# Performance work log

Hardware: AMD Instinct MI355X
Metric: run time of the kernel (lower is better)

## Reference

```python
import jax, jax.numpy as jnp
import numpy as np

NUM_HEADS = 8


def setup_inputs() -> dict:
    key = jax.random.key(0)
    ks = jax.random.split(key, 5)
    B, N, D = 2, 2048, 512
    scale = 1.0 / np.sqrt(D)  # xavier-ish init for stability
    return {
        "x": jax.random.normal(ks[0], (B, N, D), dtype=jnp.float32),
        "Wq": jax.random.normal(ks[1], (D, D), dtype=jnp.float32) * scale,
        "Wk": jax.random.normal(ks[2], (D, D), dtype=jnp.float32) * scale,
        "Wv": jax.random.normal(ks[3], (D, D), dtype=jnp.float32) * scale,
        "Wo": jax.random.normal(ks[4], (D, D), dtype=jnp.float32) * scale,
        "log_c": jnp.zeros((), dtype=jnp.float32),
        "log_beta": jnp.zeros((), dtype=jnp.float32),
    }


def reference(x, Wq, Wk, Wv, Wo, log_c, log_beta):
    B, N, D = x.shape
    H = NUM_HEADS
    dh = D // H

    # torch nn.Linear: y = x @ W.T
    def proj(W):
        return (x @ W.T).reshape(B, N, H, dh).transpose(0, 2, 1, 3)  # [B,H,N,dh]

    q, k, v = proj(Wq), proj(Wk), proj(Wv)

    c = jax.nn.softplus(log_c)
    beta = jax.nn.softplus(log_beta) + 0.5

    q_nsq = jnp.sum(q * q, axis=-1)  # [B,H,N]
    k_nsq = jnp.sum(k * k, axis=-1)  # [B,H,N]
    qk = jnp.einsum("bhnd,bhmd->bhnm", q, k)  # [B,H,N,N]

    diff_sq = jnp.maximum(q_nsq[..., :, None] - 2.0 * qk + k_nsq[..., None, :], 0.0)
    hyp_factor = jnp.sqrt(1.0 + c * (q_nsq[..., :, None] + k_nsq[..., None, :]))
    dist = jnp.sqrt(diff_sq + 1e-8) * hyp_factor
    scores = -beta * dist

    # causal mask (original: causal = mask is not None)
    causal = jnp.tril(jnp.ones((N, N), dtype=bool))
    scores = jnp.where(causal, scores, -jnp.inf)

    p = jax.nn.softmax(scores, axis=-1)
    out = jnp.einsum("bhnm,bhmd->bhnd", p, v)  # [B,H,N,dh]
    out = out.transpose(0, 2, 1, 3).reshape(B, N, D)
    return out @ Wo.T
```

## Files before the change

kernel.cpp:

```cpp
#include <hip/hip_runtime.h>
#include <math.h>

#define BB   2
#define NN   2048
#define DDIM 512
#define HH   8
#define DH   64
#define MTOT (BB*NN)
#define LDK  72
#define EE   (BB*HH*NN*DH)
#define WN   (DDIM*DDIM)
#define NSLOT (BB*HH*32*4)

typedef __attribute__((ext_vector_type(8))) short bf16x8;
typedef __attribute__((ext_vector_type(4))) float f32x4;

__device__ __forceinline__ float softplus_f(float x) {
    return x > 20.f ? x : log1pf(expf(x));
}
__device__ __forceinline__ unsigned short f2bf(float x) {
    union { float f; unsigned u; } v; v.f = x;
    unsigned r = v.u + 0x7fffu + ((v.u >> 16) & 1u);
    return (unsigned short)(r >> 16);
}
__device__ __forceinline__ float bf2f(unsigned short h) {
    union { unsigned u; float f; } v; v.u = ((unsigned)h) << 16; return v.f;
}

__global__ __launch_bounds__(256)
void split_hl(const float* __restrict__ x,  const float* __restrict__ Wq,
              const float* __restrict__ Wk, const float* __restrict__ Wv,
              const float* __restrict__ Wo,
              unsigned short* __restrict__ xh,  unsigned short* __restrict__ xl,
              unsigned short* __restrict__ wqh, unsigned short* __restrict__ wql,
              unsigned short* __restrict__ wkh, unsigned short* __restrict__ wkl,
              unsigned short* __restrict__ wvh, unsigned short* __restrict__ wvl,
              unsigned short* __restrict__ woh, unsigned short* __restrict__ wol)
{
    const float* src; unsigned short *dh, *dl; int nq;
    switch (blockIdx.y) {
        case 0:  src = x;  dh = xh;  dl = xl;  nq = EE / 4; break;
        case 1:  src = Wq; dh = wqh; dl = wql; nq = WN / 4; break;
        case 2:  src = Wk; dh = wkh; dl = wkl; nq = WN / 4; break;
        case 3:  src = Wv; dh = wvh; dl = wvl; nq = WN / 4; break;
        default: src = Wo; dh = woh; dl = wol; nq = WN / 4; break;
    }
    for (int i = blockIdx.x * 256 + threadIdx.x; i < nq; i += gridDim.x * 256) {
        float4 v = *(const float4*)(src + 4 * (size_t)i);
        ushort4 h, l;
        h.x = f2bf(v.x); l.x = f2bf(v.x - bf2f(h.x));
        h.y = f2bf(v.y); l.y = f2bf(v.y - bf2f(h.y));
        h.z = f2bf(v.z); l.z = f2bf(v.z - bf2f(h.z));
        h.w = f2bf(v.w); l.w = f2bf(v.w - bf2f(h.w));
        *(ushort4*)(dh + 4 * (size_t)i) = h;
        *(ushort4*)(dl + 4 * (size_t)i) = l;
    }
}

__global__ __launch_bounds__(256, 3)
void mm_mfma(const unsigned short* __restrict__ Ahg, const unsigned short* __restrict__ Alg,
             const unsigned short* __restrict__ W0h, const unsigned short* __restrict__ W0l,
             const unsigned short* __restrict__ W1h, const unsigned short* __restrict__ W1l,
             const unsigned short* __restrict__ W2h, const unsigned short* __restrict__ W2l,
             const int is_out,
             unsigned short* __restrict__ Qhi, unsigned short* __restrict__ Qlo,
             unsigned short* __restrict__ Khi, unsigned short* __restrict__ Klo,
             unsigned short* __restrict__ Vb, float* __restrict__ Outp,
             float* __restrict__ QN, float* __restrict__ KN)
{
    const int mode = is_out ? 3 : (int)blockIdx.z;
    const unsigned short* Wh = (mode == 1) ? W1h : ((mode == 2) ? W2h : W0h);
    const unsigned short* Wl = (mode == 1) ? W1l : ((mode == 2) ? W2l : W0l);
    const int m0 = blockIdx.x * 64, n0 = blockIdx.y * 128;

    __shared__ unsigned short Ah_s[4 * 64 * 8];
    __shared__ unsigned short Al_s[4 * 64 * 8];
    __shared__ unsigned short Bh_s[4 * 128 * 8];
    __shared__ unsigned short Bl_s[4 * 128 * 8];

    const int tid  = threadIdx.x;
    const int lane = tid & 63, lx = lane & 15, q4 = lane >> 4;
    const int w = tid >> 6, wm = w & 1, wn = w >> 1;
    const int rowA = tid & 63,  kqA = tid >> 6;
    const int rowB = tid & 127, kb  = tid >> 7;

    f32x4 acc[2][4];
    #pragma unroll
    for (int mt = 0; mt < 2; ++mt)
        #pragma unroll
        for (int nt = 0; nt < 4; ++nt)
            acc[mt][nt] = (f32x4){0.f, 0.f, 0.f, 0.f};

    const int am = m0 + rowA;
    const int ab = am >> 11, an = am & 2047;
    const size_t brow = (size_t)(n0 + rowB) * DDIM;

    uint4 rah, ral, rbh0, rbh1, rbl0, rbl1;
    {
        const int e = kqA * 8;
        size_t aoff = (mode == 3)
            ? ((((size_t)(ab * HH + (e >> 6)) * NN + an) << 6) + (e & 63))
            : ((size_t)am * DDIM + e);
        rah = *(const uint4*)(Ahg + aoff);
        ral = *(const uint4*)(Alg + aoff);
        const int eb = kb * 8;
        rbh0 = *(const uint4*)(Wh + brow + eb);
        rbh1 = *(const uint4*)(Wh + brow + eb + 16);
        rbl0 = *(const uint4*)(Wl + brow + eb);
        rbl1 = *(const uint4*)(Wl + brow + eb + 16);
    }

    for (int k0 = 0; k0 < DDIM; k0 += 32) {
        __syncthreads();
        *(uint4*)&Ah_s[(kqA << 9) + (rowA << 3)] = rah;
        *(uint4*)&Al_s[(kqA << 9) + (rowA << 3)] = ral;
        *(uint4*)&Bh_s[(kb << 10) + (rowB << 3)]       = rbh0;
        *(uint4*)&Bh_s[((kb + 2) << 10) + (rowB << 3)] = rbh1;
        *(uint4*)&Bl_s[(kb << 10) + (rowB << 3)]       = rbl0;
        *(uint4*)&Bl_s[((kb + 2) << 10) + (rowB << 3)] = rbl1;
        __syncthreads();

        if (k0 + 32 < DDIM) {
            const int e = k0 + 32 + kqA * 8;
            size_t aoff = (mode == 3)
                ? ((((size_t)(ab * HH + (e >> 6)) * NN + an) << 6) + (e & 63))
                : ((size_t)am * DDIM + e);
            rah = *(const uint4*)(Ahg + aoff);
            ral = *(const uint4*)(Alg + aoff);
            const int eb = k0 + 32 + kb * 8;
            rbh0 = *(const uint4*)(Wh + brow + eb);
            rbh1 = *(const uint4*)(Wh + brow + eb + 16);
            rbl0 = *(const uint4*)(Wl + brow + eb);
            rbl1 = *(const uint4*)(Wl + brow + eb + 16);
        }

        bf16x8 fah[2], fal[2], fbh[4], fbl[4];
        #pragma unroll
        for (int mt = 0; mt < 2; ++mt) {
            const int off = (q4 << 9) + ((wm * 32 + mt * 16 + lx) << 3);
            fah[mt] = *(const bf16x8*)&Ah_s[off];
            fal[mt] = *(const bf16x8*)&Al_s[off];
        }
        #pragma unroll
        for (int nt = 0; nt < 4; ++nt) {
            const int off = (q4 << 10) + ((wn * 64 + nt * 16 + lx) << 3);
            fbh[nt] = *(const bf16x8*)&Bh_s[off];
            fbl[nt] = *(const bf16x8*)&Bl_s[off];
        }
        #pragma unroll
        for (int mt = 0; mt < 2; ++mt)
            #pragma unroll
            for (int nt = 0; nt < 4; ++nt) {
                acc[mt][nt] = __builtin_amdgcn_mfma_f32_16x16x32_bf16(fah[mt], fbh[nt], acc[mt][nt], 0, 0, 0);
                acc[mt][nt] = __builtin_amdgcn_mfma_f32_16x16x32_bf16(fah[mt], fbl[nt], acc[mt][nt], 0, 0, 0);
                acc[mt][nt] = __builtin_amdgcn_mfma_f32_16x16x32_bf16(fal[mt], fbh[nt], acc[mt][nt], 0, 0, 0);
            }
    }

    if (mode == 0 || mode == 1) {
        float* Np = (mode == 0) ? QN : KN;
        const int head = (n0 + wn * 64) >> 6;
        #pragma unroll
        for (int mt = 0; mt < 2; ++mt)
            #pragma unroll
            for (int r = 0; r < 4; ++r) {
                float s = 0.f;
                #pragma unroll
                for (int nt = 0; nt < 4; ++nt) s = fmaf(acc[mt][nt][r], acc[mt][nt][r], s);
                s += __shfl_xor(s, 1);
                s += __shfl_xor(s, 2);
                s += __shfl_xor(s, 4);
                s += __shfl_xor(s, 8);
                if (lx == 0) {
                    const int m = m0 + wm * 32 + mt * 16 + q4 * 4 + r;
                    Np[(size_t)((m >> 11) * HH + head) * NN + (m & 2047)] = s;
                }
            }
    }

    #pragma unroll
    for (int mt = 0; mt < 2; ++mt) {
        #pragma unroll
        for (int r = 0; r < 4; ++r) {
            const int m = m0 + wm * 32 + mt * 16 + q4 * 4 + r;
            const int b = m >> 11, n2 = m & 2047;
            #pragma unroll
            for (int nt = 0; nt < 4; ++nt) {
                const int j = n0 + wn * 64 + nt * 16 + lx;
                const float v = acc[mt][nt][r];
                if (mode == 3) {
                    Outp[(size_t)m * DDIM + j] = v;
                } else {
                    const size_t idx = (((size_t)(b * HH + (j >> 6)) * NN + n2) << 6) + (j & 63);
                    if (mode == 2) {
                        Vb[idx] = f2bf(v);
                    } else {
                        const unsigned short h = f2bf(v);
                        const unsigned short l = f2bf(v - bf2f(h));
                        if (mode == 0) { Qhi[idx] = h; Qlo[idx] = l; }
                        else           { Khi[idx] = h; Klo[idx] = l; }
                    }
                }
            }
        }
    }
}

__global__ __launch_bounds__(256)
void v_transpose(const unsigned short* __restrict__ Vb, unsigned short* __restrict__ Vt)
{
    __shared__ unsigned short T[64 * LDK];
    const int id = blockIdx.x;
    const int bh = id >> 5, nt = id & 31;
    const size_t ibase = (((size_t)bh * NN + nt * 64) << 6);
    const int row = threadIdx.x >> 2, ch = threadIdx.x & 3;

    #pragma unroll
    for (int half = 0; half < 2; ++half) {
        const int col = ch * 8 + half * 32;
        *(uint4*)&T[row * LDK + col] = *(const uint4*)(Vb + ibase + (row << 6) + col);
    }
    __syncthreads();

    const size_t obase = (size_t)bh * 64 * NN;
    #pragma unroll
    for (int half = 0; half < 2; ++half) {
        const int col = ch * 8 + half * 32;
        union { unsigned short u[8]; uint4 v; } tmp;
        #pragma unroll
        for (int j = 0; j < 8; ++j) tmp.u[j] = T[(col + j) * LDK + row];
        *(uint4*)(Vt + obase + (size_t)row * NN + nt * 64 + col) = tmp.v;
    }
}

__global__ __launch_bounds__(256, 4)
void attn_mfma(const unsigned short* __restrict__ Qhi, const unsigned short* __restrict__ Qlo,
               const unsigned short* __restrict__ Khi, const unsigned short* __restrict__ Klo,
               const unsigned short* __restrict__ Vt,
               const float* __restrict__ QN, const float* __restrict__ KN,
               const float* __restrict__ pLC, const float* __restrict__ pLB,
               float* __restrict__ Opart, float* __restrict__ Mp, float* __restrict__ Lp)
{
    __shared__ unsigned short Kh_s[8 * 64 * 8];
    __shared__ unsigned short Kl_s[8 * 64 * 8];
    __shared__ unsigned short Vt_s[8 * 64 * 8];
    __shared__ unsigned short P_s [8 * 64 * 8];
    __shared__ float kn_s[64];
    __shared__ float qn_s[64];

    const int idx = blockIdx.x;
    const int g   = (idx >= 48) ? 3 : (idx >= 24) ? 2 : (idx >= 8) ? 1 : 0;
    const int rem = idx - 4 * g * (g + 1);
    const int C   = g + 1;
    const int qt  = g * 8 + rem / C;
    const int c0  = rem % C;
    const int bh  = blockIdx.y;
    const int nk  = qt + 1;
    const int kt0  = (c0 * nk) / C;
    const int kend = ((c0 + 1) * nk) / C;

    const int tid  = threadIdx.x;
    const int w    = tid >> 6;
    const int lane = tid & 63;
    const int lx   = lane & 15;
    const int q4   = lane >> 4;

    const float hc    = softplus_f(pLC[0]);
    const float betaL = (softplus_f(pLB[0]) + 0.5f) * 1.44269504f;

    const size_t base = ((size_t)bh * NN) << 6;

    union { unsigned short u[8]; bf16x8 v; } ones_u;
    #pragma unroll
    for (int j = 0; j < 8; ++j) ones_u.u[j] = 0x3F80;
    const bf16x8 ones = ones_u.v;

    const unsigned short* qrh = Qhi + base + ((size_t)(qt * 64 + w * 16 + lx) << 6) + q4 * 8;
    const unsigned short* qrl = Qlo + base + ((size_t)(qt * 64 + w * 16 + lx) << 6) + q4 * 8;
    const bf16x8 qh0 = *(const bf16x8*)(qrh);
    const bf16x8 qh1 = *(const bf16x8*)(qrh + 32);
    const bf16x8 ql0 = *(const bf16x8*)(qrl);
    const bf16x8 ql1 = *(const bf16x8*)(qrl + 32);

    if (tid < 64) qn_s[tid] = QN[(size_t)bh * NN + qt * 64 + tid];

    f32x4 Oacc[4];
    f32x4 Lacc = (f32x4){0.f, 0.f, 0.f, 0.f};
    float m_st[4];
    #pragma unroll
    for (int r = 0; r < 4; ++r) {
        m_st[r] = -INFINITY;
        Oacc[r] = (f32x4){0.f, 0.f, 0.f, 0.f};
    }

    const int srow = tid >> 2, sch = tid & 3;

    uint4 pKh0, pKh1, pKl0, pKl1, pVt0, pVt1; float pkn = 0.f;
    {
        const unsigned short* kh = Khi + base + ((size_t)(kt0 * 64 + srow) << 6);
        const unsigned short* kl = Klo + base + ((size_t)(kt0 * 64 + srow) << 6);
        const unsigned short* vt = Vt  + base + (size_t)srow * NN + kt0 * 64;
        pKh0 = *(const uint4*)(kh + sch * 8);  pKh1 = *(const uint4*)(kh + sch * 8 + 32);
        pKl0 = *(const uint4*)(kl + sch * 8);  pKl1 = *(const uint4*)(kl + sch * 8 + 32);
        pVt0 = *(const uint4*)(vt + sch * 8);  pVt1 = *(const uint4*)(vt + sch * 8 + 32);
        if (tid < 64) pkn = KN[(size_t)bh * NN + kt0 * 64 + tid];
    }

    __syncthreads();

    for (int kt = kt0; kt < kend; ++kt) {
        *(uint4*)&Kh_s[(sch << 9) + (srow << 3)]       = pKh0;
        *(uint4*)&Kh_s[((sch + 4) << 9) + (srow << 3)] = pKh1;
        *(uint4*)&Kl_s[(sch << 9) + (srow << 3)]       = pKl0;
        *(uint4*)&Kl_s[((sch + 4) << 9) + (srow << 3)] = pKl1;
        *(uint4*)&Vt_s[(sch << 9) + (srow << 3)]       = pVt0;
        *(uint4*)&Vt_s[((sch + 4) << 9) + (srow << 3)] = pVt1;
        if (tid < 64) kn_s[tid] = pkn;
        __syncthreads();

        if (kt + 1 < kend) {
            const unsigned short* kh = Khi + base + ((size_t)((kt + 1) * 64 + srow) << 6);
            const unsigned short* kl = Klo + base + ((size_t)((kt + 1) * 64 + srow) << 6);
            const unsigned short* vt = Vt  + base + (size_t)srow * NN + (kt + 1) * 64;
            pKh0 = *(const uint4*)(kh + sch * 8);  pKh1 = *(const uint4*)(kh + sch * 8 + 32);
            pKl0 = *(const uint4*)(kl + sch * 8);  pKl1 = *(const uint4*)(kl + sch * 8 + 32);
            pVt0 = *(const uint4*)(vt + sch * 8);  pVt1 = *(const uint4*)(vt + sch * 8 + 32);
            if (tid < 64) pkn = KN[(size_t)bh * NN + (kt + 1) * 64 + tid];
        }

        f32x4 S[4];
        #pragma unroll
        for (int t = 0; t < 4; ++t) {
            f32x4 acc = (f32x4){0.f, 0.f, 0.f, 0.f};
            #pragma unroll
            for (int c2 = 0; c2 < 2; ++c2) {
                const int off = ((c2 * 4 + q4) << 9) + (t << 7) + (lx << 3);
                const bf16x8 kh = *(const bf16x8*)&Kh_s[off];
                const bf16x8 kl = *(const bf16x8*)&Kl_s[off];
                const bf16x8 qh = c2 ? qh1 : qh0;
                const bf16x8 ql = c2 ? ql1 : ql0;
                acc = __builtin_amdgcn_mfma_f32_16x16x32_bf16(qh, kh, acc, 0, 0, 0);
                acc = __builtin_amdgcn_mfma_f32_16x16x32_bf16(qh, kl, acc, 0, 0, 0);
                acc = __builtin_amdgcn_mfma_f32_16x16x32_bf16(ql, kh, acc, 0, 0, 0);
            }
            S[t] = acc;
        }

        float qn_r[4];
        #pragma unroll
        for (int r = 0; r < 4; ++r) qn_r[r] = qn_s[w * 16 + q4 * 4 + r];
        const bool diag = (kt == qt);

        float mrow[4] = {-INFINITY, -INFINITY, -INFINITY, -INFINITY};
        #pragma unroll
        for (int t = 0; t < 4; ++t) {
            const float kn = kn_s[t * 16 + lx];
            #pragma unroll
            for (int r = 0; r < 4; ++r) {
                const float sumn = qn_r[r] + kn;
                float diff = fmaxf(fmaf(-2.f, S[t][r], sumn), 0.f);
                float s = -betaL * sqrtf(fmaf(hc, sumn, 1.f) * (diff + 1e-8f));
                const int cc = t * 16 + lx;
                const int rr = w * 16 + q4 * 4 + r;
                if (diag && cc > rr) s = -INFINITY;
                S[t][r] = s;
                mrow[r] = fmaxf(mrow[r], s);
            }
        }

        #pragma unroll
        for (int r = 0; r < 4; ++r) {
            float m = mrow[r];
            m = fmaxf(m, __shfl_xor(m, 1));
            m = fmaxf(m, __shfl_xor(m, 2));
            m = fmaxf(m, __shfl_xor(m, 4));
            m = fmaxf(m, __shfl_xor(m, 8));
            const float mn = fmaxf(m_st[r], m);
            const float al = exp2f(m_st[r] - mn);
            m_st[r] = mn;
            const int prow = ((w * 16 + q4 * 4 + r) << 3) + (lx & 7);
            #pragma unroll
            for (int t = 0; t < 4; ++t) {
                const float p = exp2f(S[t][r] - mn);
                P_s[((t * 2 + (lx >> 3)) << 9) + prow] = f2bf(p);
                Oacc[t][r] *= al;
            }
            Lacc[r] *= al;
        }

        __builtin_amdgcn_wave_barrier();

        #pragma unroll
        for (int c2 = 0; c2 < 2; ++c2) {
            const bf16x8 pa = *(const bf16x8*)&P_s[((c2 * 4 + q4) << 9) + ((w * 16 + lx) << 3)];
            #pragma unroll
            for (int t = 0; t < 4; ++t) {
                const bf16x8 vb = *(const bf16x8*)&Vt_s[((c2 * 4 + q4) << 9) + (t << 7) + (lx << 3)];
                Oacc[t] = __builtin_amdgcn_mfma_f32_16x16x32_bf16(pa, vb, Oacc[t], 0, 0, 0);
            }
            Lacc = __builtin_amdgcn_mfma_f32_16x16x32_bf16(pa, ones, Lacc, 0, 0, 0);
        }
        __syncthreads();
    }

    const int slot = ((bh * 32 + qt) << 2) + c0;
    float* op = Opart + ((size_t)slot << 12);
    #pragma unroll
    for (int r = 0; r < 4; ++r) {
        const int row = w * 16 + q4 * 4 + r;
        #pragma unroll
        for (int t = 0; t < 4; ++t)
            op[row * 64 + t * 16 + lx] = Oacc[t][r];
        if (lx == 0) {
            Mp[slot * 64 + row] = m_st[r];
            Lp[slot * 64 + row] = Lacc[r];
        }
    }
}

__global__ __launch_bounds__(256)
void attn_combine(const float* __restrict__ Opart, const float* __restrict__ Mp,
                  const float* __restrict__ Lp,
                  unsigned short* __restrict__ AOh, unsigned short* __restrict__ AOl)
{
    const int bh = blockIdx.x >> 5, qt = blockIdx.x & 31;
    const int C = (qt >> 3) + 1;
    const int row = threadIdx.x >> 2, qd = threadIdx.x & 3;
    const int slot0 = (bh * 32 + qt) << 2;

    float m = -INFINITY;
    for (int c = 0; c < C; ++c) m = fmaxf(m, Mp[(slot0 + c) * 64 + row]);
    float L = 0.f;
    float o[16];
    #pragma unroll
    for (int j = 0; j < 16; ++j) o[j] = 0.f;

    for (int c = 0; c < C; ++c) {
        const float wgt = exp2f(Mp[(slot0 + c) * 64 + row] - m);
        L += wgt * Lp[(slot0 + c) * 64 + row];
        const float* op = Opart + (((size_t)(slot0 + c)) << 12) + row * 64 + qd * 16;
        #pragma unroll
        for (int j4 = 0; j4 < 4; ++j4) {
            float4 v = *(const float4*)(op + j4 * 4);
            o[j4*4+0] = fmaf(wgt, v.x, o[j4*4+0]);
            o[j4*4+1] = fmaf(wgt, v.y, o[j4*4+1]);
            o[j4*4+2] = fmaf(wgt, v.z, o[j4*4+2]);
            o[j4*4+3] = fmaf(wgt, v.w, o[j4*4+3]);
        }
    }

    const float inv = 1.f / L;
    const size_t obase = (((size_t)bh * NN + qt * 64 + row) << 6) + qd * 16;
    union { unsigned short u[8]; uint4 v; } h2[2], l2[2];
    #pragma unroll
    for (int j = 0; j < 16; ++j) {
        const float ov = o[j] * inv;
        const unsigned short h = f2bf(ov);
        const unsigned short l = f2bf(ov - bf2f(h));
        h2[j >> 3].u[j & 7] = h;
        l2[j >> 3].u[j & 7] = l;
    }
    *(uint4*)(AOh + obase)     = h2[0].v;
    *(uint4*)(AOh + obase + 8) = h2[1].v;
    *(uint4*)(AOl + obase)     = l2[0].v;
    *(uint4*)(AOl + obase + 8) = l2[1].v;
}

extern "C" void kernel_launch(void* const* d_in, const int* in_sizes, int n_in,
                              void* d_out, int out_size, void* d_ws, size_t ws_size,
                              hipStream_t stream)
{
    const float* x        = (const float*)d_in[0];
    const float* Wq       = (const float*)d_in[1];
    const float* Wk       = (const float*)d_in[2];
    const float* Wv       = (const float*)d_in[3];
    const float* Wo       = (const float*)d_in[4];
    const float* log_c    = (const float*)d_in[5];
    const float* log_beta = (const float*)d_in[6];
    float* out = (float*)d_out;

    unsigned short* p = (unsigned short*)d_ws;
    unsigned short* xh  = p;            p += EE;
    unsigned short* xl  = p;            p += EE;
    unsigned short* wqh = p;            p += WN;
    unsigned short* wql = p;            p += WN;
    unsigned short* wkh = p;            p += WN;
    unsigned short* wkl = p;            p += WN;
    unsigned short* wvh = p;            p += WN;
    unsigned short* wvl = p;            p += WN;
    unsigned short* woh = p;            p += WN;
    unsigned short* wol = p;            p += WN;
    unsigned short* Qhi = p;            p += EE;
    unsigned short* Qlo = p;            p += EE;
    unsigned short* Khi = p;            p += EE;
    unsigned short* Klo = p;            p += EE;
    unsigned short* Vb  = p;            p += EE;
    unsigned short* Vtr = p;            p += EE;
    unsigned short* AOh = p;            p += EE;
    unsigned short* AOl = p;            p += EE;
    float* QN    = (float*)p;
    float* KN    = QN + (size_t)BB * HH * NN;
    float* Opart = KN + (size_t)BB * HH * NN;
    float* Mp    = Opart + (size_t)NSLOT * 64 * 64;
    float* Lp    = Mp + (size_t)NSLOT * 64;

    split_hl   <<<dim3(256, 5), 256, 0, stream>>>(x, Wq, Wk, Wv, Wo,
                                                  xh, xl, wqh, wql, wkh, wkl, wvh, wvl, woh, wol);
    mm_mfma    <<<dim3(MTOT / 64, 4, 3), 256, 0, stream>>>(xh, xl,
                                                  wqh, wql, wkh, wkl, wvh, wvl, 0,
                                                  Qhi, Qlo, Khi, Klo, Vb, nullptr, QN, KN);
    v_transpose<<<dim3(512), 256, 0, stream>>>(Vb, Vtr);
    attn_mfma  <<<dim3(80, 16), 256, 0, stream>>>(Qhi, Qlo, Khi, Klo, Vtr, QN, KN,
                                                  log_c, log_beta, Opart, Mp, Lp);
    attn_combine<<<dim3(512), 256, 0, stream>>>(Opart, Mp, Lp, AOh, AOl);
    mm_mfma    <<<dim3(MTOT / 64, 4, 1), 256, 0, stream>>>(AOh, AOl,
                                                  woh, wol, nullptr, nullptr, nullptr, nullptr, 1,
                                                  nullptr, nullptr, nullptr, nullptr, nullptr, out,
                                                  nullptr, nullptr);
}
```

Measured before the change: 220.0 us.

## Refine attention key-split grouping and narrow output projection tiles for more blocks

The attention split-K scheme now groups query tiles in sets of 4 instead of 8, giving up to 8 key chunks per tile and 144 blocks per head instead of 80. This spreads the causal workload more evenly and fills more CUs. The combine kernel is updated to the new slot indexing. The output projection GEMM is templated to use 64-wide N tiles, doubling its grid (256 to 512 blocks) for better occupancy, at the cost of more partial-result traffic and less B-tile reuse.

```diff
diff --git a/kernel.cpp b/kernel.cpp
--- a/kernel.cpp
+++ b/kernel.cpp
@@ -10,7 +10,8 @@
 #define LDK  72
 #define EE   (BB*HH*NN*DH)
 #define WN   (DDIM*DDIM)
-#define NSLOT (BB*HH*32*4)
+#define CPB  144
+#define NSLOT (BB*HH*CPB)
 
 typedef __attribute__((ext_vector_type(8))) short bf16x8;
 typedef __attribute__((ext_vector_type(4))) float f32x4;
@@ -57,6 +58,7 @@
     }
 }
 
+template<int NT>
 __global__ __launch_bounds__(256, 3)
 void mm_mfma(const unsigned short* __restrict__ Ahg, const unsigned short* __restrict__ Alg,
              const unsigned short* __restrict__ W0h, const unsigned short* __restrict__ W0l,
@@ -71,31 +73,38 @@
     const int mode = is_out ? 3 : (int)blockIdx.z;
     const unsigned short* Wh = (mode == 1) ? W1h : ((mode == 2) ? W2h : W0h);
     const unsigned short* Wl = (mode == 1) ? W1l : ((mode == 2) ? W2l : W0l);
-    const int m0 = blockIdx.x * 64, n0 = blockIdx.y * 128;
+    const int m0 = blockIdx.x * 64, n0 = blockIdx.y * NT;
+
+    constexpr int NTT = NT / 32;
+    constexpr int NW  = NT / 2;
+    constexpr int KQS = NT * 8;
 
     __shared__ unsigned short Ah_s[4 * 64 * 8];
     __shared__ unsigned short Al_s[4 * 64 * 8];
-    __shared__ unsigned short Bh_s[4 * 128 * 8];
-    __shared__ unsigned short Bl_s[4 * 128 * 8];
+    __shared__ unsigned short Bh_s[4 * NT * 8];
+    __shared__ unsigned short Bl_s[4 * NT * 8];
 
     const int tid  = threadIdx.x;
     const int lane = tid & 63, lx = lane & 15, q4 = lane >> 4;
     const int w = tid >> 6, wm = w & 1, wn = w >> 1;
-    const int rowA = tid & 63,  kqA = tid >> 6;
-    const int rowB = tid & 127, kb  = tid >> 7;
-
-    f32x4 acc[2][4];
+    const int rowA = tid & 63, kqA = tid >> 6;
+
+    int rowB, kbB;
+    if (NT == 128) { rowB = tid & 127; kbB = tid >> 7; }
+    else           { rowB = tid & 63;  kbB = tid >> 6; }
+
+    f32x4 acc[2][NTT];
     #pragma unroll
     for (int mt = 0; mt < 2; ++mt)
         #pragma unroll
-        for (int nt = 0; nt < 4; ++nt)
+        for (int nt = 0; nt < NTT; ++nt)
             acc[mt][nt] = (f32x4){0.f, 0.f, 0.f, 0.f};
 
     const int am = m0 + rowA;
     const int ab = am >> 11, an = am & 2047;
     const size_t brow = (size_t)(n0 + rowB) * DDIM;
 
-    uint4 rah, ral, rbh0, rbh1, rbl0, rbl1;
+    uint4 rah, ral, rbh0, rbl0, rbh1, rbl1;
     {
         const int e = kqA * 8;
         size_t aoff = (mode == 3)
@@ -103,21 +112,25 @@
             : ((size_t)am * DDIM + e);
         rah = *(const uint4*)(Ahg + aoff);
         ral = *(const uint4*)(Alg + aoff);
-        const int eb = kb * 8;
+        const int eb = kbB * 8;
         rbh0 = *(const uint4*)(Wh + brow + eb);
-        rbh1 = *(const uint4*)(Wh + brow + eb + 16);
         rbl0 = *(const uint4*)(Wl + brow + eb);
-        rbl1 = *(const uint4*)(Wl + brow + eb + 16);
+        if (NT == 128) {
+            rbh1 = *(const uint4*)(Wh + brow + eb + 16);
+            rbl1 = *(const uint4*)(Wl + brow + eb + 16);
+        }
     }
 
     for (int k0 = 0; k0 < DDIM; k0 += 32) {
         __syncthreads();
         *(uint4*)&Ah_s[(kqA << 9) + (rowA << 3)] = rah;
         *(uint4*)&Al_s[(kqA << 9) + (rowA << 3)] = ral;
-        *(uint4*)&Bh_s[(kb << 10) + (rowB << 3)]       = rbh0;
-        *(uint4*)&Bh_s[((kb + 2) << 10) + (rowB << 3)] = rbh1;
-        *(uint4*)&Bl_s[(kb << 10) + (rowB << 3)]       = rbl0;
-        *(uint4*)&Bl_s[((kb + 2) << 10) + (rowB << 3)] = rbl1;
+        *(uint4*)&Bh_s[kbB * KQS + (rowB << 3)] = rbh0;
+        *(uint4*)&Bl_s[kbB * KQS + (rowB << 3)] = rbl0;
+        if (NT == 128) {
+            *(uint4*)&Bh_s[(kbB + 2) * KQS + (rowB << 3)] = rbh1;
+            *(uint4*)&Bl_s[(kbB + 2) * KQS + (rowB << 3)] = rbl1;
+        }
         __syncthreads();
 
         if (k0 + 32 < DDIM) {
@@ -127,14 +140,16 @@
                 : ((size_t)am * DDIM + e);
             rah = *(const uint4*)(Ahg + aoff);
             ral = *(const uint4*)(Alg + aoff);
-            const int eb = k0 + 32 + kb * 8;
+            const int eb = k0 + 32 + kbB * 8;
             rbh0 = *(const uint4*)(Wh + brow + eb);
-            rbh1 = *(const uint4*)(Wh + brow + eb + 16);
             rbl0 = *(const uint4*)(Wl + brow + eb);
-            rbl1 = *(const uint4*)(Wl + brow + eb + 16);
-        }
-
-        bf16x8 fah[2], fal[2], fbh[4], fbl[4];
+            if (NT == 128) {
+                rbh1 = *(const uint4*)(Wh + brow + eb + 16);
+                rbl1 = *(const uint4*)(Wl + brow + eb + 16);
+            }
+        }
+
+        bf16x8 fah[2], fal[2], fbh[NTT], fbl[NTT];
         #pragma unroll
         for (int mt = 0; mt < 2; ++mt) {
             const int off = (q4 << 9) + ((wm * 32 + mt * 16 + lx) << 3);
@@ -142,22 +157,22 @@
             fal[mt] = *(const bf16x8*)&Al_s[off];
         }
         #pragma unroll
-        for (int nt = 0; nt < 4; ++nt) {
-            const int off = (q4 << 10) + ((wn * 64 + nt * 16 + lx) << 3);
+        for (int nt = 0; nt < NTT; ++nt) {
+            const int off = q4 * KQS + ((wn * NW + nt * 16 + lx) << 3);
             fbh[nt] = *(const bf16x8*)&Bh_s[off];
             fbl[nt] = *(const bf16x8*)&Bl_s[off];
         }
         #pragma unroll
         for (int mt = 0; mt < 2; ++mt)
             #pragma unroll
-            for (int nt = 0; nt < 4; ++nt) {
+            for (int nt = 0; nt < NTT; ++nt) {
                 acc[mt][nt] = __builtin_amdgcn_mfma_f32_16x16x32_bf16(fah[mt], fbh[nt], acc[mt][nt], 0, 0, 0);
                 acc[mt][nt] = __builtin_amdgcn_mfma_f32_16x16x32_bf16(fah[mt], fbl[nt], acc[mt][nt], 0, 0, 0);
                 acc[mt][nt] = __builtin_amdgcn_mfma_f32_16x16x32_bf16(fal[mt], fbh[nt], acc[mt][nt], 0, 0, 0);
             }
     }
 
-    if (mode == 0 || mode == 1) {
+    if (NT == 128 && (mode == 0 || mode == 1)) {
         float* Np = (mode == 0) ? QN : KN;
         const int head = (n0 + wn * 64) >> 6;
         #pragma unroll
@@ -166,7 +181,7 @@
             for (int r = 0; r < 4; ++r) {
                 float s = 0.f;
                 #pragma unroll
-                for (int nt = 0; nt < 4; ++nt) s = fmaf(acc[mt][nt][r], acc[mt][nt][r], s);
+                for (int nt = 0; nt < NTT; ++nt) s = fmaf(acc[mt][nt][r], acc[mt][nt][r], s);
                 s += __shfl_xor(s, 1);
                 s += __shfl_xor(s, 2);
                 s += __shfl_xor(s, 4);
@@ -185,8 +200,8 @@
             const int m = m0 + wm * 32 + mt * 16 + q4 * 4 + r;
             const int b = m >> 11, n2 = m & 2047;
             #pragma unroll
-            for (int nt = 0; nt < 4; ++nt) {
-                const int j = n0 + wn * 64 + nt * 16 + lx;
+            for (int nt = 0; nt < NTT; ++nt) {
+                const int j = n0 + wn * NW + nt * 16 + lx;
                 const float v = acc[mt][nt][r];
                 if (mode == 3) {
                     Outp[(size_t)m * DDIM + j] = v;
@@ -249,10 +264,12 @@
     __shared__ float qn_s[64];
 
     const int idx = blockIdx.x;
-    const int g   = (idx >= 48) ? 3 : (idx >= 24) ? 2 : (idx >= 8) ? 1 : 0;
-    const int rem = idx - 4 * g * (g + 1);
+    const int g   = (idx >= 112) ? 7 : (idx >= 84) ? 6 : (idx >= 60) ? 5 :
+                    (idx >= 40) ? 4 : (idx >= 24) ? 3 : (idx >= 12) ? 2 :
+                    (idx >= 4)  ? 1 : 0;
+    const int rem = idx - 2 * g * (g + 1);
     const int C   = g + 1;
-    const int qt  = g * 8 + rem / C;
+    const int qt  = g * 4 + rem / C;
     const int c0  = rem % C;
     const int bh  = blockIdx.y;
     const int nk  = qt + 1;
@@ -403,7 +420,7 @@
         __syncthreads();
     }
 
-    const int slot = ((bh * 32 + qt) << 2) + c0;
+    const int slot = bh * CPB + idx;
     float* op = Opart + ((size_t)slot << 12);
     #pragma unroll
     for (int r = 0; r < 4; ++r) {
@@ -424,9 +441,10 @@
                   unsigned short* __restrict__ AOh, unsigned short* __restrict__ AOl)
 {
     const int bh = blockIdx.x >> 5, qt = blockIdx.x & 31;
-    const int C = (qt >> 3) + 1;
+    const int g = qt >> 2, C = g + 1;
+    const int first = 2 * g * (g + 1) + (qt & 3) * C;
     const int row = threadIdx.x >> 2, qd = threadIdx.x & 3;
-    const int slot0 = (bh * 32 + qt) << 2;
+    const int slot0 = bh * CPB + first;
 
     float m = -INFINITY;
     for (int c = 0; c < C; ++c) m = fmaxf(m, Mp[(slot0 + c) * 64 + row]);
@@ -506,14 +524,14 @@
 
     split_hl   <<<dim3(256, 5), 256, 0, stream>>>(x, Wq, Wk, Wv, Wo,
                                                   xh, xl, wqh, wql, wkh, wkl, wvh, wvl, woh, wol);
-    mm_mfma    <<<dim3(MTOT / 64, 4, 3), 256, 0, stream>>>(xh, xl,
+    mm_mfma<128><<<dim3(MTOT / 64, DDIM / 128, 3), 256, 0, stream>>>(xh, xl,
                                                   wqh, wql, wkh, wkl, wvh, wvl, 0,
                                                   Qhi, Qlo, Khi, Klo, Vb, nullptr, QN, KN);
     v_transpose<<<dim3(512), 256, 0, stream>>>(Vb, Vtr);
-    attn_mfma  <<<dim3(80, 16), 256, 0, stream>>>(Qhi, Qlo, Khi, Klo, Vtr, QN, KN,
-                                                  log_c, log_beta, Opart, Mp, Lp);
+    attn_mfma  <<<dim3(CPB, 16), 256, 0, stream>>>(Qhi, Qlo, Khi, Klo, Vtr, QN, KN,
+                                                   log_c, log_beta, Opart, Mp, Lp);
     attn_combine<<<dim3(512), 256, 0, stream>>>(Opart, Mp, Lp, AOh, AOl);
-    mm_mfma    <<<dim3(MTOT / 64, 4, 1), 256, 0, stream>>>(AOh, AOl,
+    mm_mfma<64><<<dim3(MTOT / 64, DDIM / 64, 1), 256, 0, stream>>>(AOh, AOl,
                                                   woh, wol, nullptr, nullptr, nullptr, nullptr, 1,
                                                   nullptr, nullptr, nullptr, nullptr, nullptr, out,
                                                   nullptr, nullptr);
```

New measurement: 215.9 us. No clear change (-1.9%).
